# Kernel tuning notes

Hardware: AMD Instinct MI355X
Metric: run time of the kernel (lower is better)

The kernel has to match this reference:

```python
import jax, jax.numpy as jnp
import numpy as np

DIM = 384
H = 64
W = 64
NB = 8
BS = DIM // NB
WF = W // 2 + 1
EPS = 1e-5


def _layernorm(x, g, b):
    mu = jnp.mean(x, axis=-1, keepdims=True)
    var = jnp.mean(jnp.square(x - mu), axis=-1, keepdims=True)
    return (x - mu) * jax.lax.rsqrt(var + EPS) * g + b


def setup_inputs() -> dict:
    key = jax.random.key(0)
    ks = jax.random.split(key, 8)
    scale = 0.02
    x = jax.random.normal(ks[0], (8, H, W, DIM), dtype=jnp.float32)
    # complex params stored as real view (..., 2) like torch.view_as_real
    w1 = scale * jax.random.normal(ks[1], (H, WF, NB, BS, BS, 2), dtype=jnp.float32)
    b1 = scale * jax.random.normal(ks[2], (H, WF, NB, BS, 2), dtype=jnp.float32)
    norm1_w = jnp.ones((DIM,), jnp.float32)
    norm1_b = jnp.zeros((DIM,), jnp.float32)
    norm2_w = jnp.ones((DIM,), jnp.float32)
    norm2_b = jnp.zeros((DIM,), jnp.float32)
    lim1 = 1.0 / np.sqrt(DIM)
    lim2 = 1.0 / np.sqrt(4 * DIM)
    mlp_w1 = jax.random.uniform(ks[3], (DIM, 4 * DIM), jnp.float32, -lim1, lim1)
    mlp_b1 = jax.random.uniform(ks[4], (4 * DIM,), jnp.float32, -lim1, lim1)
    mlp_w2 = jax.random.uniform(ks[5], (4 * DIM, DIM), jnp.float32, -lim2, lim2)
    mlp_b2 = jax.random.uniform(ks[6], (DIM,), jnp.float32, -lim2, lim2)
    return {"x": x, "w1": w1, "b1": b1, "norm1_w": norm1_w, "norm1_b": norm1_b,
            "norm2_w": norm2_w, "norm2_b": norm2_b, "mlp_w1": mlp_w1, "mlp_b1": mlp_b1,
            "mlp_w2": mlp_w2, "mlp_b2": mlp_b2}


def reference(x, w1, b1, norm1_w, norm1_b, norm2_w, norm2_b, mlp_w1, mlp_b1, mlp_w2, mlp_b2):
    B, h, w, C = x.shape
    residual = x
    xn = _layernorm(x, norm1_w, norm1_b)
    # spectral token mixing (fp32, ortho norm)
    xf = jnp.fft.rfft2(xn.astype(jnp.float32), axes=(1, 2), norm="ortho")  # (B,H,WF,C) complex
    xf = xf.reshape(B, h, w // 2 + 1, NB, BS)
    w1c = jax.lax.complex(w1[..., 0], w1[..., 1])  # (H,WF,NB,BS,BS)
    b1c = jax.lax.complex(b1[..., 0], b1[..., 1])  # (H,WF,NB,BS)
    o1 = jnp.einsum("bhwni,hwnio->bhwno", xf, w1c) + b1c
    o1 = jax.lax.complex(jax.nn.relu(o1.real), jax.nn.relu(o1.imag))
    o1 = o1.reshape(B, h, w // 2 + 1, C)
    xs = jnp.fft.irfft2(o1, s=(h, w), axes=(1, 2), norm="ortho")  # (B,H,W,C) real
    # channel MLP (dropout in eval mode = identity), exact GELU as torch default
    xm = _layernorm(xs, norm2_w, norm2_b)
    hdn = jax.nn.gelu(xm @ mlp_w1 + mlp_b1, approximate=False)
    mlp_out = hdn @ mlp_w2 + mlp_b2
    return xs + residual + mlp_out
```

## Files before the change

### kernel.cpp

```cpp
#include <hip/hip_runtime.h>
#include <math.h>


#define BB 8
#define CC 384
#define WF 33
#define NBK 8
#define BSZ 48
#define NTOK 32768
#define TW64 0.09817477042468103f

#define T_AWF 0
#define T_AHF 5120
#define T_AHI 21504
#define T_AWI 37888

typedef __attribute__((ext_vector_type(8))) short bf16x8;
typedef __attribute__((ext_vector_type(4))) float f32x4;

__device__ __forceinline__ unsigned short f2b(float f) {
  union { float f; unsigned u; } x; x.f = f;
  unsigned u = x.u;
  return (unsigned short)((u + 0x7fffu + ((u >> 16) & 1u)) >> 16);
}
__device__ __forceinline__ float b2fl(unsigned short u) {
  return __uint_as_float(((unsigned)u) << 16);
}
__device__ __forceinline__ void gload16(const void* g, void* l) {
  __builtin_amdgcn_global_load_lds(
      (const __attribute__((address_space(1))) void*)g,
      (__attribute__((address_space(3))) void*)l, 16, 0, 0);
}

__global__ __launch_bounds__(256) void init_tw(unsigned short* __restrict__ A) {
  int idx0 = blockIdx.x * 256 + threadIdx.x;
  const float S = 0.125f;
  for (int e = idx0; e < 5120; e += 16384) {
    int m = e >> 6, w = e & 63;
    float val = 0.f;
    if (m < 66) {
      int kwv = m >> 1;
      float th = (float)((kwv * w) & 63) * TW64;
      val = (m & 1) ? (((kwv==0)||(kwv==32)) ? 0.f : -sinf(th)*S) : cosf(th)*S;
    }
    A[T_AWF + e] = f2b(val);
  }
  for (int e = idx0; e < 16384; e += 16384) {
    int comp = e >> 13; int r = e & 8191; int mp = r >> 6, hh = r & 63;
    int cpo = mp >> 6, kh = mp & 63;
    float th = (float)((kh * hh) & 63) * TW64;
    float cv = cosf(th), sv = sinf(th);
    float fv = (cpo == 0) ? (comp == 0 ? cv : sv) : (comp == 0 ? -sv : cv);
    A[T_AHF + e] = f2b(fv * S);
    float iv = (cpo == 0) ? (comp == 0 ? cv : -sv) : (comp == 0 ? sv : cv);
    A[T_AHI + e] = f2b(iv * S);
  }
  for (int e = idx0; e < 4096; e += 16384) {
    int w = e >> 6, kp = e & 63;
    float val;
    if (kp <= 32) {
      float th = (float)((kp * w) & 63) * TW64;
      val = cosf(th) * (((kp==0)||(kp==32)) ? 1.f : 2.f) * S;
    } else {
      int k2 = kp - 32;
      float th = (float)((k2 * w) & 63) * TW64;
      val = -2.f * sinf(th) * S;
    }
    A[T_AWI + e] = f2b(val);
  }
}

__global__ __launch_bounds__(256) void ln1t_kernel(const float* __restrict__ x,
    const float* __restrict__ g, const float* __restrict__ be,
    unsigned short* __restrict__ xn) {
  int outer = blockIdx.x;
  int tid = threadIdx.x, lane = tid & 63, wg = tid >> 6;
  const float* base = x + (size_t)outer * 64 * 384;
  float s[16], s2[16];
#pragma unroll
  for (int q = 0; q < 16; ++q) { s[q] = 0.f; s2[q] = 0.f; }
  for (int ch = 0; ch < 6; ++ch) {
#pragma unroll
    for (int q = 0; q < 16; ++q) {
      float v = base[(size_t)(wg*16 + q)*384 + ch*64 + lane];
      s[q] += v; s2[q] += v*v;
    }
  }
#pragma unroll
  for (int q = 0; q < 16; ++q) {
#pragma unroll
    for (int off = 32; off >= 1; off >>= 1) {
      s[q] += __shfl_xor(s[q], off);
      s2[q] += __shfl_xor(s2[q], off);
    }
  }
  float mu[16], rs[16];
#pragma unroll
  for (int q = 0; q < 16; ++q) {
    mu[q] = s[q] * (1.f/384.f);
    rs[q] = rsqrtf(s2[q] * (1.f/384.f) - mu[q]*mu[q] + 1e-5f);
  }
  unsigned short* o = xn + (size_t)outer * 384 * 64;
  for (int ch = 0; ch < 6; ++ch) {
    int c = ch*64 + lane;
    float ga = g[c], bb2 = be[c];
#pragma unroll
    for (int qq = 0; qq < 4; ++qq) {
      unsigned short hv[4];
#pragma unroll
      for (int r2 = 0; r2 < 4; ++r2) {
        int q = qq*4 + r2;
        hv[r2] = f2b((base[(size_t)(wg*16+q)*384 + c]-mu[q])*rs[q]*ga + bb2);
      }
      uint2 pw;
      pw.x = hv[0] | ((unsigned)hv[1] << 16);
      pw.y = hv[2] | ((unsigned)hv[3] << 16);
      *(uint2*)(o + (size_t)c*64 + wg*16 + qq*4) = pw;
    }
  }
}

template<int STAGE>
__global__ __launch_bounds__(256) void dft_kernel(
    const unsigned short* __restrict__ A0, const unsigned short* __restrict__ D,
    unsigned short* __restrict__ O, const float* __restrict__ xres,
    const float* __restrict__ b2, unsigned short* __restrict__ xsb,
    float* __restrict__ outp) {
  constexpr int M = (STAGE==0) ? 80 : (STAGE==3) ? 64 : 128;
  constexpr int MT = M / 16;
  constexpr int NA = (STAGE==1 || STAGE==2) ? 2 : 1;
  constexpr int ABYTES = NA * M * 128;
  constexpr int STG = ABYTES + 16384;
  constexpr int EPB = 64 * 128 * 4;
  constexpr int SB = (STG > EPB) ? STG : EPB;
  __shared__ __align__(16) char smem[SB];
  char* BPL = smem + ABYTES;

  int bid = blockIdx.x;
  int cc = bid % 3; int outer = bid / 3;
  int c0 = cc * 128;
  int tid = threadIdx.x, lane = tid & 63, wid = tid >> 6;
  int rr = lane & 15, rq = lane >> 4;
  int b, h = 0, kw = 0;
  if (STAGE == 0 || STAGE == 3) { b = outer >> 6; h = outer & 63; }
  else { b = outer / 33; kw = outer % 33; }

  f32x4 acc[MT][2];
#pragma unroll
  for (int mt = 0; mt < MT; ++mt)
#pragma unroll
    for (int nt = 0; nt < 2; ++nt) acc[mt][nt] = (f32x4){0.f,0.f,0.f,0.f};

  const unsigned short* Atab =
    (STAGE==0) ? A0+T_AWF : (STAGE==1) ? A0+T_AHF : (STAGE==2) ? A0+T_AHI : A0+T_AWI;
  constexpr int ACH = NA * M * 8;
#pragma unroll
  for (int i = 0; i < (ACH + 255)/256; ++i) {
    int t2 = tid + i*256;
    if ((ACH % 256 == 0) || (t2 < ACH)) {
      int mm = t2 >> 3, ch = t2 & 7;
      gload16(Atab + mm*64 + ((ch ^ (mm & 7)) << 3), smem + i*4096 + wid*1024);
    }
  }

  int ncomp = (STAGE == 1) ? ((kw == 0 || kw == 32) ? 1 : 2) : NA;

  for (int comp = 0; comp < ncomp; ++comp) {
    if (comp) __syncthreads();
    if (STAGE == 0) {
      const unsigned short* src = D + (((size_t)(b*64 + h))*384 + c0) * 64;
#pragma unroll
      for (int i = 0; i < 4; ++i) {
        int idx = tid + i*256;
        int c = idx >> 3, ch = idx & 7;
        gload16(src + c*64 + ((ch ^ (c & 7)) << 3), BPL + i*4096 + wid*1024);
      }
    } else {
      size_t P; int RS;
      if (STAGE == 1) { P = (size_t)b*(64*66*384) + (size_t)(2*kw + comp)*384 + c0; RS = 66*384; }
      else if (STAGE == 2) { P = ((size_t)((b*2 + comp)*33) + kw)*64*384 + c0; RS = 384; }
      else { P = (size_t)b*(64*64*384) + (size_t)h*384 + c0; RS = 64*384; }
      const unsigned short* p0 = D + P;
#pragma unroll
      for (int i = 0; i < 4; ++i) {
        int kq = (tid >> 6) + i*4;
        int c2 = (tid & 63) * 2;
        const unsigned short* p = p0 + (size_t)(4*kq)*RS + c2;
        unsigned u0 = *(const unsigned*)p;
        unsigned u1 = *(const unsigned*)(p + RS);
        unsigned u2 = *(const unsigned*)(p + 2*(size_t)RS);
        unsigned u3 = *(const unsigned*)(p + 3*(size_t)RS);
        uint2 w0, w1v;
        w0.x = (u0 & 0xffffu) | (u1 << 16);
        w0.y = (u2 & 0xffffu) | (u3 << 16);
        w1v.x = (u0 >> 16) | (u1 & 0xffff0000u);
        w1v.y = (u2 >> 16) | (u3 & 0xffff0000u);
        *(uint2*)(BPL + c2*128 + ((kq*8) ^ ((c2 & 7) << 4))) = w0;
        *(uint2*)(BPL + (c2+1)*128 + ((kq*8) ^ (((c2+1) & 7) << 4))) = w1v;
      }
    }
    __syncthreads();
#pragma unroll
    for (int kh2 = 0; kh2 < 2; ++kh2) {
      int chb = kh2*4 + rq;
      bf16x8 bfr[2];
#pragma unroll
      for (int nt = 0; nt < 2; ++nt) {
        int n = wid*32 + nt*16 + rr;
        bfr[nt] = *(const bf16x8*)(BPL + n*128 + ((chb ^ (n & 7)) << 4));
      }
#pragma unroll
      for (int mt = 0; mt < MT; ++mt) {
        int mr = mt*16 + rr;
        bf16x8 af = *(const bf16x8*)(smem + comp*(M*128) + mr*128 + ((chb ^ (mr & 7)) << 4));
#pragma unroll
        for (int nt = 0; nt < 2; ++nt)
          acc[mt][nt] = __builtin_amdgcn_mfma_f32_16x16x32_bf16(af, bfr[nt], acc[mt][nt], 0, 0, 0);
      }
    }
  }
  __syncthreads();

  float* ep = (float*)smem;
  constexpr int NHM = (M + 63) / 64;
#pragma unroll
  for (int hm = 0; hm < NHM; ++hm) {
    if (hm) __syncthreads();
    constexpr int span = 4;
#pragma unroll
    for (int mo = 0; mo < span; ++mo) {
      int mt = hm*4 + mo;
      if (mt >= MT) break;
#pragma unroll
      for (int nt = 0; nt < 2; ++nt)
#pragma unroll
        for (int j = 0; j < 4; ++j) {
          int m2 = mo*16 + rq*4 + j;
          int cl = wid*32 + nt*16 + rr;
          ep[m2*128 + (cl ^ ((m2 & 7) << 2))] = acc[mt][nt][j];
        }
    }
    __syncthreads();
    if (STAGE < 3) {
      for (int it = tid; it < 64*16; it += 256) {
        int m2 = it >> 4, u8 = it & 15;
        int m = hm*64 + m2;
        if (m >= M) break;
        if (STAGE == 0 && m >= 66) break;
        if (STAGE == 2) { int cp = m >> 6; if (cp && (kw == 0 || kw == 32)) continue; }
        int swz = (m2 & 7) << 2;
        float4 v0 = *(const float4*)(ep + m2*128 + ((u8*8) ^ swz));
        float4 v1 = *(const float4*)(ep + m2*128 + ((u8*8 + 4) ^ swz));
        uint4 pw;
        pw.x = f2b(v0.x) | ((unsigned)f2b(v0.y) << 16);
        pw.y = f2b(v0.z) | ((unsigned)f2b(v0.w) << 16);
        pw.z = f2b(v1.x) | ((unsigned)f2b(v1.y) << 16);
        pw.w = f2b(v1.z) | ((unsigned)f2b(v1.w) << 16);
        size_t rowb;
        if (STAGE == 0) rowb = ((size_t)(b*64 + h)*66 + m)*384 + c0;
        else if (STAGE == 1) { int cp = m >> 6, kh = m & 63;
          rowb = (((size_t)((b*2 + cp)*64 + kh)*33) + kw)*384 + c0; }
        else { int cp = m >> 6, h2 = m & 63; int kp = cp ? 32 + kw : kw;
          rowb = ((size_t)(b*64 + kp)*64 + h2)*384 + c0; }
        *(uint4*)(O + rowb + u8*8) = pw;
      }
    } else {
      for (int it = tid; it < 64*32; it += 256) {
        int m = it >> 5, u = it & 31;
        int swz = (m & 7) << 2;
        float4 v = *(const float4*)(ep + m*128 + ((u*4) ^ swz));
        size_t idx = ((size_t)(b*64 + h)*64 + m)*384 + c0 + u*4;
        float4 rx = *(const float4*)(xres + idx);
        float4 ov;
        ov.x = v.x + rx.x + b2[c0 + u*4 + 0];
        ov.y = v.y + rx.y + b2[c0 + u*4 + 1];
        ov.z = v.z + rx.z + b2[c0 + u*4 + 2];
        ov.w = v.w + rx.w + b2[c0 + u*4 + 3];
        *(float4*)(outp + idx) = ov;
      }
      for (int it = tid; it < 64*16; it += 256) {
        int m = it >> 4, u8 = it & 15;
        int swz = (m & 7) << 2;
        float4 v0 = *(const float4*)(ep + m*128 + ((u8*8) ^ swz));
        float4 v1 = *(const float4*)(ep + m*128 + ((u8*8 + 4) ^ swz));
        uint4 pw;
        pw.x = f2b(v0.x) | ((unsigned)f2b(v0.y) << 16);
        pw.y = f2b(v0.z) | ((unsigned)f2b(v0.w) << 16);
        pw.z = f2b(v1.x) | ((unsigned)f2b(v1.y) << 16);
        pw.w = f2b(v1.z) | ((unsigned)f2b(v1.w) << 16);
        *(uint4*)(xsb + ((size_t)(b*64 + h)*64 + m)*384 + c0 + u8*8) = pw;
      }
    }
  }
}

__global__ __launch_bounds__(384) void blockmm2_kernel(
    const unsigned short* __restrict__ S2, const float* __restrict__ w1,
    const float* __restrict__ b1, unsigned short* __restrict__ o1) {
  int bid = blockIdx.x;
  int n = bid % NBK;
  int kw = (bid / NBK) % WF;
  int h = bid / (NBK*WF);
  int tid = threadIdx.x;
  __shared__ float2 wl[BSZ*BSZ];
  __shared__ float2 xl2[BB][BSZ];
  __shared__ float2 bl[BSZ];
  const float2* wbase = (const float2*)w1 + ((size_t)(h*WF + kw)*NBK + n)*(BSZ*BSZ);
  for (int t = tid; t < BSZ*BSZ; t += 384) wl[t] = wbase[t];
  const float2* bbase = (const float2*)b1 + ((size_t)(h*WF + kw)*NBK + n)*BSZ;
  if (tid < BSZ) bl[tid] = bbase[tid];
  {
    int bb = tid / BSZ, i = tid % BSZ;
    size_t ir = (((size_t)((bb*2 + 0)*64 + h)*33) + kw)*384 + n*48 + i;
    size_t ii = (((size_t)((bb*2 + 1)*64 + h)*33) + kw)*384 + n*48 + i;
    xl2[bb][i] = make_float2(b2fl(S2[ir]), b2fl(S2[ii]));
  }
  __syncthreads();
  int bb = tid / BSZ, o = tid % BSZ;
  float2 acc = bl[o];
#pragma unroll
  for (int i = 0; i < BSZ; ++i) {
    float2 xv = xl2[bb][i];
    float2 wv = wl[i*BSZ + o];
    acc.x += xv.x*wv.x - xv.y*wv.y;
    acc.y += xv.x*wv.y + xv.y*wv.x;
  }
  size_t idr = (((size_t)((bb*2 + 0)*33) + kw)*64 + h)*384 + n*48 + o;
  size_t idi = (((size_t)((bb*2 + 1)*33) + kw)*64 + h)*384 + n*48 + o;
  o1[idr] = f2b(fmaxf(acc.x, 0.f));
  o1[idi] = f2b(fmaxf(acc.y, 0.f));
}

__global__ __launch_bounds__(256) void ln2_kernel(const unsigned short* __restrict__ in,
    const float* __restrict__ g, const float* __restrict__ bsh,
    unsigned short* __restrict__ outp) {
  int token = blockIdx.x * 4 + (threadIdx.x >> 6);
  int lane = threadIdx.x & 63;
  const unsigned short* row = in + (size_t)token * CC;
  float v[6]; float s = 0.f;
#pragma unroll
  for (int j = 0; j < 6; ++j) { v[j] = b2fl(row[lane + 64*j]); s += v[j]; }
#pragma unroll
  for (int off = 32; off >= 1; off >>= 1) s += __shfl_xor(s, off);
  float mu = s * (1.0f/CC);
  float q = 0.f;
#pragma unroll
  for (int j = 0; j < 6; ++j) { float d = v[j] - mu; q += d*d; }
#pragma unroll
  for (int off = 32; off >= 1; off >>= 1) q += __shfl_xor(q, off);
  float rs = rsqrtf(q * (1.0f/CC) + 1e-5f);
#pragma unroll
  for (int j = 0; j < 6; ++j) {
    int c = lane + 64*j;
    outp[(size_t)token*CC + c] = f2b((v[j]-mu)*rs*g[c] + bsh[c]);
  }
}

__global__ __launch_bounds__(256) void convtr_kernel(const float* __restrict__ in,
    unsigned short* __restrict__ out, int R, int C) {
  __shared__ float tile[32][33];
  int ntc = C >> 5;
  int bx = blockIdx.x % ntc;
  int by = blockIdx.x / ntc;
  int tx = threadIdx.x & 31, ty = threadIdx.x >> 5;
  for (int rr2 = ty; rr2 < 32; rr2 += 8)
    tile[rr2][tx] = in[(size_t)(by*32+rr2)*C + bx*32 + tx];
  __syncthreads();
  for (int rr2 = ty; rr2 < 32; rr2 += 8)
    out[(size_t)(bx*32+rr2)*R + by*32 + tx] = f2b(tile[tx][rr2]);
}

template<int GELU, int OUTBF16>
__global__ __launch_bounds__(256) void mfma_gemm_kernel(
    const unsigned short* __restrict__ A, int lda,
    const unsigned short* __restrict__ BT, int ldbt,
    const float* __restrict__ bias,
    void* __restrict__ Cp, int ldc, int K, int ntn) {
  __shared__ __align__(16) unsigned short gsm[128*64*2];
  unsigned short* As = gsm;
  unsigned short* Bs = gsm + 128*64;
  int bn = blockIdx.x % ntn;
  int bm = blockIdx.x / ntn;
  int t = threadIdx.x;
  int lane = t & 63;
  int wid = t >> 6;
  int wm = wid >> 1, wn = wid & 1;
  int rr = lane & 15, rq = lane >> 4;

  f32x4 acc[4][4];
#pragma unroll
  for (int m = 0; m < 4; ++m)
#pragma unroll
    for (int n = 0; n < 4; ++n) acc[m][n] = (f32x4){0.f,0.f,0.f,0.f};

  const unsigned short* Abase = A + (size_t)bm*128*lda;
  const unsigned short* Bbase = BT + (size_t)bn*128*ldbt;

  for (int k0 = 0; k0 < K; k0 += 64) {
#pragma unroll
    for (int i = 0; i < 4; ++i) {
      int idx = t + i*256;
      int row = idx >> 3, ch = idx & 7;
      gload16(Abase + (size_t)row*lda + k0 + ((ch ^ (row & 7)) << 3),
              (char*)As + i*4096 + wid*1024);
    }
#pragma unroll
    for (int i = 0; i < 4; ++i) {
      int idx = t + i*256;
      int row = idx >> 3, ch = idx & 7;
      gload16(Bbase + (size_t)row*ldbt + k0 + ((ch ^ (row & 7)) << 3),
              (char*)Bs + i*4096 + wid*1024);
    }
    __syncthreads();
#pragma unroll
    for (int ks = 0; ks < 2; ++ks) {
      int chb = ks*4 + rq;
      bf16x8 af[4], bfr[4];
#pragma unroll
      for (int m = 0; m < 4; ++m) {
        int row = wm*64 + m*16 + rr;
        af[m] = *(const bf16x8*)((const char*)As + row*128 + ((chb ^ (row & 7)) << 4));
      }
#pragma unroll
      for (int n = 0; n < 4; ++n) {
        int row = wn*64 + n*16 + rr;
        bfr[n] = *(const bf16x8*)((const char*)Bs + row*128 + ((chb ^ (row & 7)) << 4));
      }
#pragma unroll
      for (int m = 0; m < 4; ++m)
#pragma unroll
        for (int n = 0; n < 4; ++n)
          acc[m][n] = __builtin_amdgcn_mfma_f32_16x16x32_bf16(af[m], bfr[n], acc[m][n], 0, 0, 0);
    }
    __syncthreads();
  }

  if (OUTBF16) {
    unsigned short* ep = gsm;
#pragma unroll
    for (int m = 0; m < 4; ++m)
#pragma unroll
      for (int n = 0; n < 4; ++n)
#pragma unroll
        for (int j = 0; j < 4; ++j) {
          int row = wm*64 + m*16 + rq*4 + j;
          int col = wn*64 + n*16 + rr;
          float v = acc[m][n][j];
          if (GELU) {
            v += bias[bn*128 + col];
            v = 0.5f*v*(1.f + erff(v*0.70710678118654752f));
          }
          ep[row*128 + (col ^ ((row & 7) << 3))] = f2b(v);
        }
    __syncthreads();
    for (int it = t; it < 128*16; it += 256) {
      int m = it >> 4, u8 = it & 15;
      uint4 pw = *(const uint4*)(ep + m*128 + ((u8*8) ^ ((m & 7) << 3)));
      *(uint4*)((unsigned short*)Cp + (size_t)(bm*128 + m)*ldc + bn*128 + u8*8) = pw;
    }
  } else {
#pragma unroll
    for (int m = 0; m < 4; ++m) {
#pragma unroll
      for (int n = 0; n < 4; ++n) {
        int grow0 = bm*128 + wm*64 + m*16 + rq*4;
        int gcol  = bn*128 + wn*64 + n*16 + rr;
#pragma unroll
        for (int j = 0; j < 4; ++j) {
          float v = acc[m][n][j];
          if (GELU) { v += bias[gcol]; v = 0.5f*v*(1.f + erff(v*0.70710678118654752f)); }
          ((float*)Cp)[(size_t)(grow0+j)*ldc + gcol] += v;
        }
      }
    }
  }
}

extern "C" void kernel_launch(void* const* d_in, const int* in_sizes, int n_in,
                              void* d_out, int out_size, void* d_ws, size_t ws_size,
                              hipStream_t stream) {
  const float* x   = (const float*)d_in[0];
  const float* w1  = (const float*)d_in[1];
  const float* b1  = (const float*)d_in[2];
  const float* n1w = (const float*)d_in[3];
  const float* n1b = (const float*)d_in[4];
  const float* n2w = (const float*)d_in[5];
  const float* n2b = (const float*)d_in[6];
  const float* mw1 = (const float*)d_in[7];
  const float* mb1 = (const float*)d_in[8];
  const float* mw2 = (const float*)d_in[9];
  const float* mb2 = (const float*)d_in[10];
  float* out = (float*)d_out;

  char* ws = (char*)d_ws;
  const size_t MB = 1ull << 20;
  unsigned short* xn  = (unsigned short*)(ws + 0*MB);
  unsigned short* S1  = (unsigned short*)(ws + 26*MB);
  unsigned short* S2  = (unsigned short*)(ws + 53*MB);
  unsigned short* o1  = (unsigned short*)(ws + 80*MB);
  unsigned short* S3  = (unsigned short*)(ws + 107*MB);
  unsigned short* xsb = (unsigned short*)(ws + 133*MB);
  unsigned short* xmb = (unsigned short*)(ws + 159*MB);
  unsigned short* hid = (unsigned short*)(ws + 185*MB);
  unsigned short* w1t = (unsigned short*)(ws + 286*MB);
  unsigned short* w2t = (unsigned short*)(ws + 288*MB);
  unsigned short* atab = (unsigned short*)(ws + 290*MB);

  init_tw<<<64, 256, 0, stream>>>(atab);
  convtr_kernel<<<(384/32)*(1536/32), 256, 0, stream>>>(mw1, w1t, 384, 1536);
  convtr_kernel<<<(1536/32)*(384/32), 256, 0, stream>>>(mw2, w2t, 1536, 384);

  ln1t_kernel<<<512, 256, 0, stream>>>(x, n1w, n1b, xn);
  dft_kernel<0><<<512*3, 256, 0, stream>>>(atab, xn, S1, nullptr, nullptr, nullptr, nullptr);
  dft_kernel<1><<<264*3, 256, 0, stream>>>(atab, S1, S2, nullptr, nullptr, nullptr, nullptr);
  blockmm2_kernel<<<64*WF*NBK, 384, 0, stream>>>(S2, w1, b1, o1);
  dft_kernel<2><<<264*3, 256, 0, stream>>>(atab, o1, S3, nullptr, nullptr, nullptr, nullptr);
  dft_kernel<3><<<512*3, 256, 0, stream>>>(atab, S3, nullptr, x, mb2, xsb, out);
  ln2_kernel<<<NTOK/4, 256, 0, stream>>>(xsb, n2w, n2b, xmb);
  mfma_gemm_kernel<1,1><<<256*12, 256, 0, stream>>>(xmb, 384, w1t, 384, mb1,
                                                    hid, 1536, 384, 12);
  mfma_gemm_kernel<0,0><<<256*3, 256, 0, stream>>>(hid, 1536, w2t, 1536, nullptr,
                                                   out, 384, 1536, 3);
}
```

Before: 406.7 us.

## Fuse residual epilogue into MLP GEMM, merge prep kernels, widen block-MM work

The last DFT stage no longer writes the fp32 output with residual and bias. The second MLP GEMM now writes the final output directly, adding x, the bf16 spectral output and the bias in a coalesced LDS-staged epilogue instead of a read-modify-write of the output. The twiddle-table init and the two weight transposes are merged into one prep launch. The block-diagonal complex matmul now has each block handle two channel blocks with two outputs per thread, and the GEMM adds a block-index swizzle for cache locality. The residual add now uses the bf16-rounded spectral output, which slightly lowers precision.

```diff
diff --git a/kernel.cpp b/kernel.cpp
--- a/kernel.cpp
+++ b/kernel.cpp
@@ -32,42 +32,61 @@
       (__attribute__((address_space(3))) void*)l, 16, 0, 0);
 }
 
-__global__ __launch_bounds__(256) void init_tw(unsigned short* __restrict__ A) {
-  int idx0 = blockIdx.x * 256 + threadIdx.x;
-  const float S = 0.125f;
-  for (int e = idx0; e < 5120; e += 16384) {
-    int m = e >> 6, w = e & 63;
-    float val = 0.f;
-    if (m < 66) {
-      int kwv = m >> 1;
-      float th = (float)((kwv * w) & 63) * TW64;
-      val = (m & 1) ? (((kwv==0)||(kwv==32)) ? 0.f : -sinf(th)*S) : cosf(th)*S;
-    }
-    A[T_AWF + e] = f2b(val);
-  }
-  for (int e = idx0; e < 16384; e += 16384) {
-    int comp = e >> 13; int r = e & 8191; int mp = r >> 6, hh = r & 63;
-    int cpo = mp >> 6, kh = mp & 63;
-    float th = (float)((kh * hh) & 63) * TW64;
-    float cv = cosf(th), sv = sinf(th);
-    float fv = (cpo == 0) ? (comp == 0 ? cv : sv) : (comp == 0 ? -sv : cv);
-    A[T_AHF + e] = f2b(fv * S);
-    float iv = (cpo == 0) ? (comp == 0 ? cv : -sv) : (comp == 0 ? sv : cv);
-    A[T_AHI + e] = f2b(iv * S);
-  }
-  for (int e = idx0; e < 4096; e += 16384) {
-    int w = e >> 6, kp = e & 63;
-    float val;
-    if (kp <= 32) {
-      float th = (float)((kp * w) & 63) * TW64;
-      val = cosf(th) * (((kp==0)||(kp==32)) ? 1.f : 2.f) * S;
-    } else {
-      int k2 = kp - 32;
-      float th = (float)((k2 * w) & 63) * TW64;
-      val = -2.f * sinf(th) * S;
-    }
-    A[T_AWI + e] = f2b(val);
-  }
+__global__ __launch_bounds__(256) void prep_kernel(unsigned short* __restrict__ A,
+    const float* __restrict__ mw1, unsigned short* __restrict__ w1t,
+    const float* __restrict__ mw2, unsigned short* __restrict__ w2t) {
+  __shared__ float tile[32][33];
+  int bid = blockIdx.x;
+  if (bid < 64) {
+    int idx0 = bid * 256 + threadIdx.x;
+    const float S = 0.125f;
+    for (int e = idx0; e < 5120; e += 16384) {
+      int m = e >> 6, w = e & 63;
+      float val = 0.f;
+      if (m < 66) {
+        int kwv = m >> 1;
+        float th = (float)((kwv * w) & 63) * TW64;
+        val = (m & 1) ? (((kwv==0)||(kwv==32)) ? 0.f : -sinf(th)*S) : cosf(th)*S;
+      }
+      A[T_AWF + e] = f2b(val);
+    }
+    for (int e = idx0; e < 16384; e += 16384) {
+      int comp = e >> 13; int r = e & 8191; int mp = r >> 6, hh = r & 63;
+      int cpo = mp >> 6, kh = mp & 63;
+      float th = (float)((kh * hh) & 63) * TW64;
+      float cv = cosf(th), sv = sinf(th);
+      float fv = (cpo == 0) ? (comp == 0 ? cv : sv) : (comp == 0 ? -sv : cv);
+      A[T_AHF + e] = f2b(fv * S);
+      float iv = (cpo == 0) ? (comp == 0 ? cv : -sv) : (comp == 0 ? sv : cv);
+      A[T_AHI + e] = f2b(iv * S);
+    }
+    for (int e = idx0; e < 4096; e += 16384) {
+      int w = e >> 6, kp = e & 63;
+      float val;
+      if (kp <= 32) {
+        float th = (float)((kp * w) & 63) * TW64;
+        val = cosf(th) * (((kp==0)||(kp==32)) ? 1.f : 2.f) * S;
+      } else {
+        int k2 = kp - 32;
+        float th = (float)((k2 * w) & 63) * TW64;
+        val = -2.f * sinf(th) * S;
+      }
+      A[T_AWI + e] = f2b(val);
+    }
+    return;
+  }
+  const float* in; unsigned short* outb; int R, C, tb;
+  if (bid < 640) { in = mw1; outb = w1t; R = 384; C = 1536; tb = bid - 64; }
+  else           { in = mw2; outb = w2t; R = 1536; C = 384; tb = bid - 640; }
+  int ntc = C >> 5;
+  int bx = tb % ntc;
+  int by = tb / ntc;
+  int tx = threadIdx.x & 31, ty = threadIdx.x >> 5;
+  for (int rr2 = ty; rr2 < 32; rr2 += 8)
+    tile[rr2][tx] = in[(size_t)(by*32+rr2)*C + bx*32 + tx];
+  __syncthreads();
+  for (int rr2 = ty; rr2 < 32; rr2 += 8)
+    outb[(size_t)(bx*32+rr2)*R + by*32 + tx] = f2b(tile[tx][rr2]);
 }
 
 __global__ __launch_bounds__(256) void ln1t_kernel(const float* __restrict__ x,
@@ -123,9 +142,7 @@
 template<int STAGE>
 __global__ __launch_bounds__(256) void dft_kernel(
     const unsigned short* __restrict__ A0, const unsigned short* __restrict__ D,
-    unsigned short* __restrict__ O, const float* __restrict__ xres,
-    const float* __restrict__ b2, unsigned short* __restrict__ xsb,
-    float* __restrict__ outp) {
+    unsigned short* __restrict__ O) {
   constexpr int M = (STAGE==0) ? 80 : (STAGE==3) ? 64 : 128;
   constexpr int MT = M / 16;
   constexpr int NA = (STAGE==1 || STAGE==2) ? 2 : 1;
@@ -226,9 +243,8 @@
 #pragma unroll
   for (int hm = 0; hm < NHM; ++hm) {
     if (hm) __syncthreads();
-    constexpr int span = 4;
-#pragma unroll
-    for (int mo = 0; mo < span; ++mo) {
+#pragma unroll
+    for (int mo = 0; mo < 4; ++mo) {
       int mt = hm*4 + mo;
       if (mt >= MT) break;
 #pragma unroll
@@ -241,55 +257,28 @@
         }
     }
     __syncthreads();
-    if (STAGE < 3) {
-      for (int it = tid; it < 64*16; it += 256) {
-        int m2 = it >> 4, u8 = it & 15;
-        int m = hm*64 + m2;
-        if (m >= M) break;
-        if (STAGE == 0 && m >= 66) break;
-        if (STAGE == 2) { int cp = m >> 6; if (cp && (kw == 0 || kw == 32)) continue; }
-        int swz = (m2 & 7) << 2;
-        float4 v0 = *(const float4*)(ep + m2*128 + ((u8*8) ^ swz));
-        float4 v1 = *(const float4*)(ep + m2*128 + ((u8*8 + 4) ^ swz));
-        uint4 pw;
-        pw.x = f2b(v0.x) | ((unsigned)f2b(v0.y) << 16);
-        pw.y = f2b(v0.z) | ((unsigned)f2b(v0.w) << 16);
-        pw.z = f2b(v1.x) | ((unsigned)f2b(v1.y) << 16);
-        pw.w = f2b(v1.z) | ((unsigned)f2b(v1.w) << 16);
-        size_t rowb;
-        if (STAGE == 0) rowb = ((size_t)(b*64 + h)*66 + m)*384 + c0;
-        else if (STAGE == 1) { int cp = m >> 6, kh = m & 63;
-          rowb = (((size_t)((b*2 + cp)*64 + kh)*33) + kw)*384 + c0; }
-        else { int cp = m >> 6, h2 = m & 63; int kp = cp ? 32 + kw : kw;
-          rowb = ((size_t)(b*64 + kp)*64 + h2)*384 + c0; }
-        *(uint4*)(O + rowb + u8*8) = pw;
-      }
-    } else {
-      for (int it = tid; it < 64*32; it += 256) {
-        int m = it >> 5, u = it & 31;
-        int swz = (m & 7) << 2;
-        float4 v = *(const float4*)(ep + m*128 + ((u*4) ^ swz));
-        size_t idx = ((size_t)(b*64 + h)*64 + m)*384 + c0 + u*4;
-        float4 rx = *(const float4*)(xres + idx);
-        float4 ov;
-        ov.x = v.x + rx.x + b2[c0 + u*4 + 0];
-        ov.y = v.y + rx.y + b2[c0 + u*4 + 1];
-        ov.z = v.z + rx.z + b2[c0 + u*4 + 2];
-        ov.w = v.w + rx.w + b2[c0 + u*4 + 3];
-        *(float4*)(outp + idx) = ov;
-      }
-      for (int it = tid; it < 64*16; it += 256) {
-        int m = it >> 4, u8 = it & 15;
-        int swz = (m & 7) << 2;
-        float4 v0 = *(const float4*)(ep + m*128 + ((u8*8) ^ swz));
-        float4 v1 = *(const float4*)(ep + m*128 + ((u8*8 + 4) ^ swz));
-        uint4 pw;
-        pw.x = f2b(v0.x) | ((unsigned)f2b(v0.y) << 16);
-        pw.y = f2b(v0.z) | ((unsigned)f2b(v0.w) << 16);
-        pw.z = f2b(v1.x) | ((unsigned)f2b(v1.y) << 16);
-        pw.w = f2b(v1.z) | ((unsigned)f2b(v1.w) << 16);
-        *(uint4*)(xsb + ((size_t)(b*64 + h)*64 + m)*384 + c0 + u8*8) = pw;
-      }
+    for (int it = tid; it < 64*16; it += 256) {
+      int m2 = it >> 4, u8 = it & 15;
+      int m = hm*64 + m2;
+      if (m >= M) break;
+      if (STAGE == 0 && m >= 66) break;
+      if (STAGE == 2) { int cp = m >> 6; if (cp && (kw == 0 || kw == 32)) continue; }
+      int swz = (m2 & 7) << 2;
+      float4 v0 = *(const float4*)(ep + m2*128 + ((u8*8) ^ swz));
+      float4 v1 = *(const float4*)(ep + m2*128 + ((u8*8 + 4) ^ swz));
+      uint4 pw;
+      pw.x = f2b(v0.x) | ((unsigned)f2b(v0.y) << 16);
+      pw.y = f2b(v0.z) | ((unsigned)f2b(v0.w) << 16);
+      pw.z = f2b(v1.x) | ((unsigned)f2b(v1.y) << 16);
+      pw.w = f2b(v1.z) | ((unsigned)f2b(v1.w) << 16);
+      size_t rowb;
+      if (STAGE == 0) rowb = ((size_t)(b*64 + h)*66 + m)*384 + c0;
+      else if (STAGE == 1) { int cp = m >> 6, kh = m & 63;
+        rowb = (((size_t)((b*2 + cp)*64 + kh)*33) + kw)*384 + c0; }
+      else if (STAGE == 2) { int cp = m >> 6, h2 = m & 63; int kp = cp ? 32 + kw : kw;
+        rowb = ((size_t)(b*64 + kp)*64 + h2)*384 + c0; }
+      else rowb = ((size_t)(b*64 + h)*64 + m)*384 + c0;
+      *(uint4*)(O + rowb + u8*8) = pw;
     }
   }
 }
@@ -298,37 +287,50 @@
     const unsigned short* __restrict__ S2, const float* __restrict__ w1,
     const float* __restrict__ b1, unsigned short* __restrict__ o1) {
   int bid = blockIdx.x;
-  int n = bid % NBK;
-  int kw = (bid / NBK) % WF;
-  int h = bid / (NBK*WF);
+  int np = bid % 4;
+  int kw = (bid / 4) % WF;
+  int h = bid / (4*WF);
   int tid = threadIdx.x;
-  __shared__ float2 wl[BSZ*BSZ];
-  __shared__ float2 xl2[BB][BSZ];
-  __shared__ float2 bl[BSZ];
-  const float2* wbase = (const float2*)w1 + ((size_t)(h*WF + kw)*NBK + n)*(BSZ*BSZ);
-  for (int t = tid; t < BSZ*BSZ; t += 384) wl[t] = wbase[t];
-  const float2* bbase = (const float2*)b1 + ((size_t)(h*WF + kw)*NBK + n)*BSZ;
-  if (tid < BSZ) bl[tid] = bbase[tid];
-  {
-    int bb = tid / BSZ, i = tid % BSZ;
+  __shared__ float4 wl4[2][48*24];
+  __shared__ float2 xl[2][BB][48];
+  __shared__ float2 bl[2][48];
+#pragma unroll
+  for (int e = tid; e < 2304; e += 384) {
+    int sub = e / 1152, r = e % 1152;
+    const float4* wb4 = (const float4*)(w1 + ((size_t)((h*WF + kw)*NBK) + 2*np + sub)*(BSZ*BSZ*2));
+    wl4[sub][r] = wb4[r];
+  }
+  if (tid < 96) {
+    int sub = tid / 48, o = tid % 48;
+    bl[sub][o] = ((const float2*)b1)[((size_t)((h*WF + kw)*NBK) + 2*np + sub)*BSZ + o];
+  }
+#pragma unroll
+  for (int e = tid; e < 768; e += 384) {
+    int sub = e / 384, r = e % 384, bb = r / 48, i = r % 48;
+    int n = 2*np + sub;
     size_t ir = (((size_t)((bb*2 + 0)*64 + h)*33) + kw)*384 + n*48 + i;
     size_t ii = (((size_t)((bb*2 + 1)*64 + h)*33) + kw)*384 + n*48 + i;
-    xl2[bb][i] = make_float2(b2fl(S2[ir]), b2fl(S2[ii]));
+    xl[sub][bb][i] = make_float2(b2fl(S2[ir]), b2fl(S2[ii]));
   }
   __syncthreads();
-  int bb = tid / BSZ, o = tid % BSZ;
-  float2 acc = bl[o];
-#pragma unroll
-  for (int i = 0; i < BSZ; ++i) {
-    float2 xv = xl2[bb][i];
-    float2 wv = wl[i*BSZ + o];
-    acc.x += xv.x*wv.x - xv.y*wv.y;
-    acc.y += xv.x*wv.y + xv.y*wv.x;
-  }
-  size_t idr = (((size_t)((bb*2 + 0)*33) + kw)*64 + h)*384 + n*48 + o;
-  size_t idi = (((size_t)((bb*2 + 1)*33) + kw)*64 + h)*384 + n*48 + o;
-  o1[idr] = f2b(fmaxf(acc.x, 0.f));
-  o1[idi] = f2b(fmaxf(acc.y, 0.f));
+  int sub = tid / 192, r = tid % 192, bb = r / 24, o2 = r % 24;
+  float4 bv = *(const float4*)(&bl[sub][2*o2]);
+  float2 a0 = make_float2(bv.x, bv.y);
+  float2 a1 = make_float2(bv.z, bv.w);
+#pragma unroll
+  for (int i = 0; i < 48; ++i) {
+    float2 xv = xl[sub][bb][i];
+    float4 wv = wl4[sub][i*24 + o2];
+    a0.x += xv.x*wv.x - xv.y*wv.y;
+    a0.y += xv.x*wv.y + xv.y*wv.x;
+    a1.x += xv.x*wv.z - xv.y*wv.w;
+    a1.y += xv.x*wv.w + xv.y*wv.z;
+  }
+  int n = 2*np + sub;
+  size_t idr = (((size_t)((bb*2 + 0)*33) + kw)*64 + h)*384 + n*48 + 2*o2;
+  size_t idi = (((size_t)((bb*2 + 1)*33) + kw)*64 + h)*384 + n*48 + 2*o2;
+  *(unsigned*)(o1 + idr) = f2b(fmaxf(a0.x, 0.f)) | ((unsigned)f2b(fmaxf(a1.x, 0.f)) << 16);
+  *(unsigned*)(o1 + idi) = f2b(fmaxf(a0.y, 0.f)) | ((unsigned)f2b(fmaxf(a1.y, 0.f)) << 16);
 }
 
 __global__ __launch_bounds__(256) void ln2_kernel(const unsigned short* __restrict__ in,
@@ -356,31 +358,22 @@
   }
 }
 
-__global__ __launch_bounds__(256) void convtr_kernel(const float* __restrict__ in,
-    unsigned short* __restrict__ out, int R, int C) {
-  __shared__ float tile[32][33];
-  int ntc = C >> 5;
-  int bx = blockIdx.x % ntc;
-  int by = blockIdx.x / ntc;
-  int tx = threadIdx.x & 31, ty = threadIdx.x >> 5;
-  for (int rr2 = ty; rr2 < 32; rr2 += 8)
-    tile[rr2][tx] = in[(size_t)(by*32+rr2)*C + bx*32 + tx];
-  __syncthreads();
-  for (int rr2 = ty; rr2 < 32; rr2 += 8)
-    out[(size_t)(bx*32+rr2)*R + by*32 + tx] = f2b(tile[tx][rr2]);
-}
-
-template<int GELU, int OUTBF16>
+template<int MODE>
 __global__ __launch_bounds__(256) void mfma_gemm_kernel(
     const unsigned short* __restrict__ A, int lda,
     const unsigned short* __restrict__ BT, int ldbt,
     const float* __restrict__ bias,
-    void* __restrict__ Cp, int ldc, int K, int ntn) {
+    void* __restrict__ Cp, int ldc, int K, int ntn,
+    const unsigned short* __restrict__ xsb, const float* __restrict__ xres,
+    const float* __restrict__ b2v) {
   __shared__ __align__(16) unsigned short gsm[128*64*2];
   unsigned short* As = gsm;
   unsigned short* Bs = gsm + 128*64;
-  int bn = blockIdx.x % ntn;
-  int bm = blockIdx.x / ntn;
+  int nb = (int)gridDim.x;
+  int bidx = (int)blockIdx.x;
+  int bswz = (bidx & 7) * (nb >> 3) + (bidx >> 3);
+  int bn = bswz % ntn;
+  int bm = bswz / ntn;
   int t = threadIdx.x;
   int lane = t & 63;
   int wid = t >> 6;
@@ -435,7 +428,7 @@
     __syncthreads();
   }
 
-  if (OUTBF16) {
+  if (MODE == 0) {
     unsigned short* ep = gsm;
 #pragma unroll
     for (int m = 0; m < 4; ++m)
@@ -446,10 +439,8 @@
           int row = wm*64 + m*16 + rq*4 + j;
           int col = wn*64 + n*16 + rr;
           float v = acc[m][n][j];
-          if (GELU) {
-            v += bias[bn*128 + col];
-            v = 0.5f*v*(1.f + erff(v*0.70710678118654752f));
-          }
+          v += bias[bn*128 + col];
+          v = 0.5f*v*(1.f + erff(v*0.70710678118654752f));
           ep[row*128 + (col ^ ((row & 7) << 3))] = f2b(v);
         }
     __syncthreads();
@@ -459,18 +450,39 @@
       *(uint4*)((unsigned short*)Cp + (size_t)(bm*128 + m)*ldc + bn*128 + u8*8) = pw;
     }
   } else {
-#pragma unroll
-    for (int m = 0; m < 4; ++m) {
-#pragma unroll
-      for (int n = 0; n < 4; ++n) {
-        int grow0 = bm*128 + wm*64 + m*16 + rq*4;
-        int gcol  = bn*128 + wn*64 + n*16 + rr;
-#pragma unroll
-        for (int j = 0; j < 4; ++j) {
-          float v = acc[m][n][j];
-          if (GELU) { v += bias[gcol]; v = 0.5f*v*(1.f + erff(v*0.70710678118654752f)); }
-          ((float*)Cp)[(size_t)(grow0+j)*ldc + gcol] += v;
-        }
+    float* ep = (float*)gsm;
+#pragma unroll
+    for (int half = 0; half < 2; ++half) {
+      __syncthreads();
+#pragma unroll
+      for (int mo = 0; mo < 2; ++mo) {
+        int m = half*2 + mo;
+#pragma unroll
+        for (int n = 0; n < 4; ++n)
+#pragma unroll
+          for (int j = 0; j < 4; ++j) {
+            int lr = wm*32 + mo*16 + rq*4 + j;
+            int col = wn*64 + n*16 + rr;
+            ep[lr*128 + (col ^ ((lr & 7) << 2))] = acc[m][n][j];
+          }
+      }
+      __syncthreads();
+      for (int it = t; it < 64*32; it += 256) {
+        int lr = it >> 5, u = it & 31;
+        int swz = (lr & 7) << 2;
+        float4 v = *(const float4*)(ep + lr*128 + ((u*4) ^ swz));
+        int grow = bm*128 + (lr >> 5)*64 + (half*2 + ((lr >> 4) & 1))*16 + (lr & 15);
+        int gcol = bn*128 + u*4;
+        size_t idx = (size_t)grow*ldc + gcol;
+        float4 xr = *(const float4*)(xres + idx);
+        uint2 xsv = *(const uint2*)(xsb + idx);
+        float4 bv = *(const float4*)(b2v + gcol);
+        float4 ov;
+        ov.x = v.x + xr.x + b2fl((unsigned short)(xsv.x & 0xffffu)) + bv.x;
+        ov.y = v.y + xr.y + b2fl((unsigned short)(xsv.x >> 16)) + bv.y;
+        ov.z = v.z + xr.z + b2fl((unsigned short)(xsv.y & 0xffffu)) + bv.z;
+        ov.w = v.w + xr.w + b2fl((unsigned short)(xsv.y >> 16)) + bv.w;
+        *(float4*)((float*)Cp + idx) = ov;
       }
     }
   }
@@ -506,19 +518,19 @@
   unsigned short* w2t = (unsigned short*)(ws + 288*MB);
   unsigned short* atab = (unsigned short*)(ws + 290*MB);
 
-  init_tw<<<64, 256, 0, stream>>>(atab);
-  convtr_kernel<<<(384/32)*(1536/32), 256, 0, stream>>>(mw1, w1t, 384, 1536);
-  convtr_kernel<<<(1536/32)*(384/32), 256, 0, stream>>>(mw2, w2t, 1536, 384);
+  prep_kernel<<<1216, 256, 0, stream>>>(atab, mw1, w1t, mw2, w2t);
 
   ln1t_kernel<<<512, 256, 0, stream>>>(x, n1w, n1b, xn);
-  dft_kernel<0><<<512*3, 256, 0, stream>>>(atab, xn, S1, nullptr, nullptr, nullptr, nullptr);
-  dft_kernel<1><<<264*3, 256, 0, stream>>>(atab, S1, S2, nullptr, nullptr, nullptr, nullptr);
-  blockmm2_kernel<<<64*WF*NBK, 384, 0, stream>>>(S2, w1, b1, o1);
-  dft_kernel<2><<<264*3, 256, 0, stream>>>(atab, o1, S3, nullptr, nullptr, nullptr, nullptr);
-  dft_kernel<3><<<512*3, 256, 0, stream>>>(atab, S3, nullptr, x, mb2, xsb, out);
+  dft_kernel<0><<<512*3, 256, 0, stream>>>(atab, xn, S1);
+  dft_kernel<1><<<264*3, 256, 0, stream>>>(atab, S1, S2);
+  blockmm2_kernel<<<64*WF*4, 384, 0, stream>>>(S2, w1, b1, o1);
+  dft_kernel<2><<<264*3, 256, 0, stream>>>(atab, o1, S3);
+  dft_kernel<3><<<512*3, 256, 0, stream>>>(atab, S3, xsb);
   ln2_kernel<<<NTOK/4, 256, 0, stream>>>(xsb, n2w, n2b, xmb);
-  mfma_gemm_kernel<1,1><<<256*12, 256, 0, stream>>>(xmb, 384, w1t, 384, mb1,
-                                                    hid, 1536, 384, 12);
-  mfma_gemm_kernel<0,0><<<256*3, 256, 0, stream>>>(hid, 1536, w2t, 1536, nullptr,
-                                                   out, 384, 1536, 3);
-}
+  mfma_gemm_kernel<0><<<256*12, 256, 0, stream>>>(xmb, 384, w1t, 384, mb1,
+                                                  hid, 1536, 384, 12,
+                                                  nullptr, nullptr, nullptr);
+  mfma_gemm_kernel<1><<<256*3, 256, 0, stream>>>(hid, 1536, w2t, 1536, nullptr,
+                                                 out, 384, 1536, 3,
+                                                 xsb, x, mb2);
+}
```

Result: faster. 386.3 us (-5.0%).
